# Kernel tuning notes

Hardware: AMD Instinct MI355X
Metric: run time of the kernel (lower is better)

## Reference

```python
import jax, jax.numpy as jnp
import numpy as np

B, N, D, H, DK, MS, FF = 8, 256, 256, 16, 16, 16, 512
EPS = 1e-5


def _inorm(x, scale, bias):
    # InstanceNorm1d over the node dim (axis=1) per channel, affine
    m = jnp.mean(x, axis=1, keepdims=True)
    v = jnp.var(x, axis=1, keepdims=True)
    return (x - m) * jax.lax.rsqrt(v + EPS) * scale + bias


def _heads(x):
    b, n, _ = x.shape
    return x.reshape(b, n, H, DK).transpose(0, 2, 1, 3)  # (b,H,n,DK)


def _block(emb_r, emb_c, cost, Wq, Wk, Wv, m1w, m1b, m2w, m2b, cw, cb,
           n1s, n1b, w1, b1, w2, b2, n2s, n2b):
    b, n, _ = emb_r.shape
    q = _heads(emb_r @ Wq)
    k = _heads(emb_c @ Wk)
    v = _heads(emb_c @ Wv)
    dot = jnp.einsum('bhid,bhjd->bhij', q, k) / jnp.sqrt(jnp.float32(DK))
    # stack dot-product score with cost-matrix score: (b,H,r,c,2)
    two = jnp.stack([dot, jnp.broadcast_to(cost[:, None], dot.shape)], axis=-1)
    # per-head 2 -> MS -> 1 MLP on each (row,col) score pair
    ms1 = jax.nn.relu(jnp.einsum('bhrcs,hsm->bhrcm', two, m1w)
                      + m1b[None, :, None, None, :])
    mixed = jnp.einsum('bhrcm,hm->bhrc', ms1, m2w[:, :, 0]) \
            + m2b[:, 0][None, :, None, None]
    w = jax.nn.softmax(mixed, axis=-1)
    out = jnp.einsum('bhrc,bhcd->bhrd', w, v)
    out_concat = out.transpose(0, 2, 1, 3).reshape(b, n, H * DK)
    mh = out_concat @ cw + cb
    out1 = _inorm(emb_r + mh, n1s, n1b)
    ff = jax.nn.relu(out1 @ w1 + b1) @ w2 + b2
    return _inorm(out1 + ff, n2s, n2b)


def setup_inputs() -> dict:
    key = jax.random.key(0)
    keys = iter(jax.random.split(key, 64))
    def nrm(shape, s=0.05):
        return jax.random.normal(next(keys), shape, dtype=jnp.float32) * s
    inp = {
        'row_emb': nrm((B, N, D), 1.0),
        'col_emb': nrm((B, N, D), 1.0),
        'cost_mat': jax.random.uniform(next(keys), (B, N, N), dtype=jnp.float32),
    }
    for p in ('r', 'c'):
        inp[p + 'Wq'] = nrm((D, H * DK)); inp[p + 'Wk'] = nrm((D, H * DK)); inp[p + 'Wv'] = nrm((D, H * DK))
        inp[p + 'm1w'] = nrm((H, 2, MS), 0.5); inp[p + 'm1b'] = nrm((H, MS), 0.5)
        inp[p + 'm2w'] = nrm((H, MS, 1), 0.25); inp[p + 'm2b'] = nrm((H, 1), 0.25)
        inp[p + 'cw'] = nrm((H * DK, D)); inp[p + 'cb'] = jnp.zeros((D,), jnp.float32)
        inp[p + 'n1s'] = jnp.ones((D,), jnp.float32); inp[p + 'n1b'] = jnp.zeros((D,), jnp.float32)
        inp[p + 'w1'] = nrm((D, FF)); inp[p + 'b1'] = jnp.zeros((FF,), jnp.float32)
        inp[p + 'w2'] = nrm((FF, D)); inp[p + 'b2'] = jnp.zeros((D,), jnp.float32)
        inp[p + 'n2s'] = jnp.ones((D,), jnp.float32); inp[p + 'n2b'] = jnp.zeros((D,), jnp.float32)
    return inp


def reference(row_emb, col_emb, cost_mat,
              rWq, rWk, rWv, rm1w, rm1b, rm2w, rm2b, rcw, rcb,
              rn1s, rn1b, rw1, rb1, rw2, rb2, rn2s, rn2b,
              cWq, cWk, cWv, cm1w, cm1b, cm2w, cm2b, ccw, ccb,
              cn1s, cn1b, cw1, cb1, cw2, cb2, cn2s, cn2b):
    row_out = _block(row_emb, col_emb, cost_mat,
                     rWq, rWk, rWv, rm1w, rm1b, rm2w, rm2b, rcw, rcb,
                     rn1s, rn1b, rw1, rb1, rw2, rb2, rn2s, rn2b)
    col_out = _block(col_emb, row_emb, cost_mat.transpose(0, 2, 1),
                     cWq, cWk, cWv, cm1w, cm1b, cm2w, cm2b, ccw, ccb,
                     cn1s, cn1b, cw1, cb1, cw2, cb2, cn2s, cn2b)
    return row_out, col_out
```

## Files before the change

kernel.cpp:

```cpp
#include <hip/hip_runtime.h>
#include <hip/hip_bf16.h>
#include <hip/hip_fp16.h>

#define Bc 8
#define Nc 256
#define Dc 256
#define Hc 16
#define DKc 16
#define MSc 16
#define FFc 512
#define SZc 524288
#define WHALF 524288
#define FFH 1048576

typedef __hip_bfloat16 bf16;
typedef __attribute__((ext_vector_type(8))) short bfrag8;
typedef __attribute__((ext_vector_type(4))) float f32x4;

__device__ __forceinline__ short f2bs(float x) {
    bf16 t = __float2bfloat16(x);
    return *reinterpret_cast<short*>(&t);
}

__device__ __forceinline__ short f2hs(float x) {
    __half t = __float2half(x);
    return *reinterpret_cast<short*>(&t);
}

__device__ __forceinline__ __half2 pk_relu(__half2 x) {
    __half2 r;
    asm("v_pk_max_f16 %0, %1, 0" : "=v"(r) : "v"(x));
    return r;
}

__global__ void setup_kernel(const float* __restrict__ e0, const float* __restrict__ e1,
                             bf16* __restrict__ o0, bf16* __restrict__ o1,
                             float* __restrict__ statsB,
                             const float* __restrict__ cost,
                             short* __restrict__ costH, short* __restrict__ costHT,
                             const float* rWq, const float* rWk, const float* rWv,
                             const float* rcw, const float* rw1, const float* rw2,
                             const float* cWq, const float* cWk, const float* cWv,
                             const float* ccw, const float* cw1, const float* cw2,
                             const float* rm1w, const float* rm1b, const float* rm2w,
                             const float* cm1w, const float* cm1b, const float* cm2w,
                             __half2* __restrict__ Wpk,
                             bf16* __restrict__ WT) {
    int y = blockIdx.y;
    if (y < 2) {
        const float* src = y ? e1 : e0;
        bf16* dst = y ? o1 : o0;
        size_t base = (size_t)blockIdx.x * 2048 + threadIdx.x;
#pragma unroll
        for (int i = 0; i < 8; ++i)
            dst[base + i * 256] = __float2bfloat16(src[base + i * 256]);
        return;
    }
    if (y == 2) {
        if (blockIdx.x < 64) {
            statsB[blockIdx.x * 256 + threadIdx.x] = 0.f;
        } else if (blockIdx.x < 66) {
            int p = blockIdx.x - 64;
            const float* m1w = p ? cm1w : rm1w;
            const float* m1b = p ? cm1b : rm1b;
            const float* m2w = p ? cm2w : rm2w;
            int h = threadIdx.x >> 4, m = threadIdx.x & 15;
            __half2* wp = Wpk + (size_t)(p * 16 + h) * 64;
            wp[m]      = __float2half2_rn(m1w[h * 32 + m] * 0.25f);
            wp[16 + m] = __float2half2_rn(m1w[h * 32 + 16 + m]);
            wp[32 + m] = __float2half2_rn(m1b[h * 16 + m]);
            wp[48 + m] = __float2half2_rn(m2w[h * 16 + m]);
        }
        return;
    }
    if (y == 15) {
        size_t base = (size_t)blockIdx.x * 2048 + threadIdx.x;
#pragma unroll
        for (int i = 0; i < 8; ++i)
            costH[base + i * 256] = f2hs(cost[base + i * 256]);
        return;
    }
    __shared__ float t[32][33];
    int tx = threadIdx.x & 31, ty = threadIdx.x >> 5;
    if (y >= 16) {
        int tl = blockIdx.x + (y - 16) * 256;
        int bb = tl >> 6, t2 = tl & 63;
        int r0 = (t2 >> 3) * 32, c0 = (t2 & 7) * 32;
        const float* src = cost + (size_t)bb * 65536;
        short* dst = costHT + (size_t)bb * 65536;
#pragma unroll
        for (int i = 0; i < 4; ++i)
            t[ty + i * 8][tx] = src[(size_t)(r0 + ty + i * 8) * 256 + c0 + tx];
        __syncthreads();
#pragma unroll
        for (int i = 0; i < 4; ++i)
            dst[(size_t)(c0 + ty + i * 8) * 256 + r0 + tx] = f2hs(t[tx][ty + i * 8]);
        return;
    }
    int z = y - 3;
    int p = z / 6, widx = z % 6;
    const float* src; int K, N; size_t off;
    switch (widx) {
        case 0: src = p ? cWq : rWq; K = 256; N = 256; off = 0; break;
        case 1: src = p ? cWk : rWk; K = 256; N = 256; off = 65536; break;
        case 2: src = p ? cWv : rWv; K = 256; N = 256; off = 131072; break;
        case 3: src = p ? ccw : rcw; K = 256; N = 256; off = 196608; break;
        case 4: src = p ? cw1 : rw1; K = 256; N = 512; off = 262144; break;
        default: src = p ? cw2 : rw2; K = 512; N = 256; off = 393216; break;
    }
    int Ntiles = N >> 5, Ktiles = K >> 5;
    if ((int)blockIdx.x >= Ktiles * Ntiles) return;
    int kt = blockIdx.x / Ntiles, nt = blockIdx.x - kt * Ntiles;
    int k0 = kt * 32, n0 = nt * 32;
    bf16* dst = WT + (size_t)p * WHALF + off;
#pragma unroll
    for (int i = 0; i < 4; ++i)
        t[ty + i * 8][tx] = src[(size_t)(k0 + ty + i * 8) * N + n0 + tx];
    __syncthreads();
#pragma unroll
    for (int i = 0; i < 4; ++i)
        dst[(size_t)(n0 + ty + i * 8) * K + k0 + tx] = __float2bfloat16(t[tx][ty + i * 8]);
}

__global__ void gemm_qkv_kernel(const short* __restrict__ embRb, const short* __restrict__ embCb,
                                const short* __restrict__ WT, bf16* __restrict__ qkv) {
    int z = blockIdx.z;
    int p = z / 3, j = z % 3;
    const short* A  = (j == 0) ? (p ? embCb : embRb) : (p ? embRb : embCb);
    const short* BT = WT + (size_t)p * WHALF + j * 65536;
    bf16* out = qkv + (size_t)z * SZc;

    int lane = threadIdx.x & 63, w = threadIdx.x >> 6;
    int m_base = blockIdx.x * 64 + (w & 1) * 32;
    int n_base = blockIdx.y * 64 + (w >> 1) * 32;
    int mr = lane & 15, quad = lane >> 4;

    const short* pa0 = A + (size_t)(m_base + mr) * 256 + quad * 8;
    const short* pa1 = pa0 + 16 * 256;
    const short* pb0 = BT + (size_t)(n_base + mr) * 256 + quad * 8;
    const short* pb1 = pb0 + 16 * 256;

    f32x4 acc00 = {0.f, 0.f, 0.f, 0.f}, acc01 = {0.f, 0.f, 0.f, 0.f};
    f32x4 acc10 = {0.f, 0.f, 0.f, 0.f}, acc11 = {0.f, 0.f, 0.f, 0.f};
#pragma unroll
    for (int kt = 0; kt < 256; kt += 32) {
        bfrag8 A0 = *(const bfrag8*)(pa0 + kt);
        bfrag8 A1 = *(const bfrag8*)(pa1 + kt);
        bfrag8 B0 = *(const bfrag8*)(pb0 + kt);
        bfrag8 B1 = *(const bfrag8*)(pb1 + kt);
        acc00 = __builtin_amdgcn_mfma_f32_16x16x32_bf16(A0, B0, acc00, 0, 0, 0);
        acc01 = __builtin_amdgcn_mfma_f32_16x16x32_bf16(A0, B1, acc01, 0, 0, 0);
        acc10 = __builtin_amdgcn_mfma_f32_16x16x32_bf16(A1, B0, acc10, 0, 0, 0);
        acc11 = __builtin_amdgcn_mfma_f32_16x16x32_bf16(A1, B1, acc11, 0, 0, 0);
    }

#pragma unroll
    for (int jt = 0; jt < 2; ++jt) {
        int col = n_base + jt * 16 + mr;
        int h = col >> 4, dk = col & 15;
        f32x4 a0 = jt ? acc01 : acc00;
        f32x4 a1 = jt ? acc11 : acc10;
#pragma unroll
        for (int r = 0; r < 4; ++r) {
            int row0 = m_base + quad * 4 + r;
            int row1 = row0 + 16;
            int b0 = row0 >> 8, n0 = row0 & 255;
            int b1 = row1 >> 8, n1 = row1 & 255;
            out[((size_t)(b0 * Hc + h) * Nc + n0) * DKc + dk] = __float2bfloat16(a0[r]);
            out[((size_t)(b1 * Hc + h) * Nc + n1) * DKc + dk] = __float2bfloat16(a1[r]);
        }
    }
}

__global__ void attn_kernel(const short* __restrict__ qkv,
                            const short* __restrict__ costH,
                            const short* __restrict__ costHT,
                            const __half2* __restrict__ Wpk,
                            const float* rm2b, const float* cm2b,
                            bf16* __restrict__ attnb) {
    int b = blockIdx.x, h = blockIdx.y;
    int p = blockIdx.z >> 4, rc = blockIdx.z & 15;
    const short* Q = qkv + (size_t)(p * 3 + 0) * SZc;
    const short* K = qkv + (size_t)(p * 3 + 1) * SZc;
    const short* V = qkv + (size_t)(p * 3 + 2) * SZc;
    const __half2* wp = Wpk + (size_t)(p * 16 + h) * 64;
    float b2v = (p ? cm2b : rm2b)[h];
    bf16* out_concat = attnb + (size_t)p * SZc;

    int bh = b * Hc + h;
    int r0 = rc * 16;
    int c = threadIdx.x;
    int lane = c & 63, wid = c >> 6;
    int mr = lane & 15, quad = lane >> 4;

    __shared__ __align__(16) short sVT[16 * 264];
    __shared__ __align__(16) short sEb[16 * 264];
    __shared__ float sPart[4 * 256];
    __shared__ float sSum[16 * 4];

    {
        const short* vp = V + ((size_t)bh * Nc + c) * DKc;
        bfrag8 v0 = *(const bfrag8*)vp;
        bfrag8 v1 = *(const bfrag8*)(vp + 8);
#pragma unroll
        for (int i = 0; i < 8; ++i) {
            sVT[i * 264 + c]       = v0[i];
            sVT[(8 + i) * 264 + c] = v1[i];
        }
    }

    bfrag8 qf = {0, 0, 0, 0, 0, 0, 0, 0};
    if (quad < 2)
        qf = *(const bfrag8*)(Q + ((size_t)bh * Nc + r0 + mr) * DKc + quad * 8);

    __half2 sv2[8];
#pragma unroll
    for (int t = 0; t < 4; ++t) {
        bfrag8 kf = {0, 0, 0, 0, 0, 0, 0, 0};
        if (quad < 2)
            kf = *(const bfrag8*)(K + ((size_t)bh * Nc + wid * 64 + t * 16 + mr) * DKc + quad * 8);
        f32x4 acc = {0.f, 0.f, 0.f, 0.f};
        acc = __builtin_amdgcn_mfma_f32_16x16x32_bf16(qf, kf, acc, 0, 0, 0);
        sv2[t * 2]     = __floats2half2_rn(acc[0], acc[1]);
        sv2[t * 2 + 1] = __floats2half2_rn(acc[2], acc[3]);
    }

    const __half2* cp = (const __half2*)((p ? costH : costHT) + (size_t)b * 65536);
    __half2 cv2[8];
#pragma unroll
    for (int t = 0; t < 4; ++t) {
        int col = wid * 64 + t * 16 + mr;
        int h2i = (col << 7) + (r0 >> 1) + (quad << 1);
        uint2 u = *(const uint2*)(cp + h2i);
        cv2[t * 2]     = *reinterpret_cast<__half2*>(&u.x);
        cv2[t * 2 + 1] = *reinterpret_cast<__half2*>(&u.y);
    }

    __syncthreads();

    const __half2 z2 = __half2half2(__float2half(0.f));
    __half2 mix2[8] = {z2, z2, z2, z2, z2, z2, z2, z2};
#pragma unroll
    for (int m = 0; m < MSc; ++m) {
        __half2 w1d = wp[m];
        __half2 w1c = wp[16 + m];
        __half2 b1v = wp[32 + m];
        __half2 w2v = wp[48 + m];
#pragma unroll
        for (int s = 0; s < 8; ++s) {
            __half2 tt = __hfma2(sv2[s], w1d, __hfma2(cv2[s], w1c, b1v));
            mix2[s] = __hfma2(pk_relu(tt), w2v, mix2[s]);
        }
    }
    float ex[16];
#pragma unroll
    for (int s = 0; s < 8; ++s) {
        float2 mf = __half22float2(mix2[s]);
        ex[s * 2]     = __expf(mf.x + b2v);
        ex[s * 2 + 1] = __expf(mf.y + b2v);
    }

#pragma unroll
    for (int t = 0; t < 4; ++t)
#pragma unroll
        for (int r = 0; r < 4; ++r)
            sEb[(quad * 4 + r) * 264 + wid * 64 + t * 16 + mr] = f2bs(ex[t * 4 + r]);

#pragma unroll
    for (int r = 0; r < 4; ++r) {
        float rp = ex[r] + ex[4 + r] + ex[8 + r] + ex[12 + r];
        rp += __shfl_xor(rp, 1);
        rp += __shfl_xor(rp, 2);
        rp += __shfl_xor(rp, 4);
        rp += __shfl_xor(rp, 8);
        if (mr == 0) sSum[(quad * 4 + r) * 4 + wid] = rp;
    }
    __syncthreads();

    {
        const short* pa = &sEb[mr * 264 + wid * 64 + quad * 8];
        const short* pb = &sVT[mr * 264 + wid * 64 + quad * 8];
        f32x4 acc = {0.f, 0.f, 0.f, 0.f};
        bfrag8 a0 = *(const bfrag8*)pa;
        bfrag8 b0 = *(const bfrag8*)pb;
        acc = __builtin_amdgcn_mfma_f32_16x16x32_bf16(a0, b0, acc, 0, 0, 0);
        bfrag8 a1 = *(const bfrag8*)(pa + 32);
        bfrag8 b1 = *(const bfrag8*)(pb + 32);
        acc = __builtin_amdgcn_mfma_f32_16x16x32_bf16(a1, b1, acc, 0, 0, 0);
#pragma unroll
        for (int r = 0; r < 4; ++r)
            sPart[wid * 256 + (quad * 4 + r) * 16 + mr] = acc[r];
    }
    __syncthreads();

    {
        int r = c >> 4, dk = c & 15;
        float o = sPart[c] + sPart[256 + c] + sPart[512 + c] + sPart[768 + c];
        float sum = sSum[r * 4] + sSum[r * 4 + 1] + sSum[r * 4 + 2] + sSum[r * 4 + 3];
        out_concat[((size_t)(b * Nc + r0 + r)) * Dc + h * DKc + dk] =
            __float2bfloat16(o / sum);
    }
}

__global__ void gemm_cat_kernel(const short* __restrict__ attnb, const short* __restrict__ WT,
                                const float* rcb, const float* ccb,
                                const float* __restrict__ resR, const float* __restrict__ resC,
                                float* __restrict__ x1, float* __restrict__ stats1) {
    int p = blockIdx.z;
    const short* A  = attnb + (size_t)p * SZc;
    const short* BT = WT + (size_t)p * WHALF + 196608;
    const float* bias = p ? ccb : rcb;
    const float* res  = p ? resC : resR;
    float* outF = x1 + (size_t)p * SZc;
    float* st   = stats1 + p * 4096;

    int lane = threadIdx.x & 63, w = threadIdx.x >> 6;
    int m_base = blockIdx.x * 64 + (w & 1) * 32;
    int n_base = blockIdx.y * 64 + (w >> 1) * 32;
    int mr = lane & 15, quad = lane >> 4;

    const short* pa0 = A + (size_t)(m_base + mr) * 256 + quad * 8;
    const short* pa1 = pa0 + (size_t)16 * 256;
    const short* pb0 = BT + (size_t)(n_base + mr) * 256 + quad * 8;
    const short* pb1 = pb0 + (size_t)16 * 256;

    f32x4 acc00 = {0.f, 0.f, 0.f, 0.f}, acc01 = {0.f, 0.f, 0.f, 0.f};
    f32x4 acc10 = {0.f, 0.f, 0.f, 0.f}, acc11 = {0.f, 0.f, 0.f, 0.f};
#pragma unroll
    for (int kt = 0; kt < 256; kt += 32) {
        bfrag8 A0 = *(const bfrag8*)(pa0 + kt);
        bfrag8 A1 = *(const bfrag8*)(pa1 + kt);
        bfrag8 B0 = *(const bfrag8*)(pb0 + kt);
        bfrag8 B1 = *(const bfrag8*)(pb1 + kt);
        acc00 = __builtin_amdgcn_mfma_f32_16x16x32_bf16(A0, B0, acc00, 0, 0, 0);
        acc01 = __builtin_amdgcn_mfma_f32_16x16x32_bf16(A0, B1, acc01, 0, 0, 0);
        acc10 = __builtin_amdgcn_mfma_f32_16x16x32_bf16(A1, B0, acc10, 0, 0, 0);
        acc11 = __builtin_amdgcn_mfma_f32_16x16x32_bf16(A1, B1, acc11, 0, 0, 0);
    }

    int bb = m_base >> 8;
#pragma unroll
    for (int jt = 0; jt < 2; ++jt) {
        int col = n_base + jt * 16 + mr;
        float bv = bias[col];
        f32x4 a0 = jt ? acc01 : acc00;
        f32x4 a1 = jt ? acc11 : acc10;
        float ssum = 0.f, ssq = 0.f;
#pragma unroll
        for (int r = 0; r < 4; ++r) {
            int row0 = m_base + quad * 4 + r;
            int row1 = row0 + 16;
            float v0 = a0[r] + bv + res[(size_t)row0 * 256 + col];
            float v1 = a1[r] + bv + res[(size_t)row1 * 256 + col];
            outF[(size_t)row0 * 256 + col] = v0;
            outF[(size_t)row1 * 256 + col] = v1;
            ssum += v0 + v1;
            ssq  += v0 * v0 + v1 * v1;
        }
        atomicAdd(&st[(bb * 256 + col) * 2],     ssum);
        atomicAdd(&st[(bb * 256 + col) * 2 + 1], ssq);
    }
}

__global__ __launch_bounds__(256) void gemm_ff1n_kernel(
        const float* __restrict__ x1, const float* __restrict__ stats1,
        const float* rn1s, const float* rn1b, const float* cn1s, const float* cn1b,
        const short* __restrict__ WT, const float* rb1, const float* cb1,
        bf16* __restrict__ ffh) {
    int p = blockIdx.z;
    const float* X   = x1 + (size_t)p * SZc;
    const float* st  = stats1 + p * 4096;
    const float* n1s = p ? cn1s : rn1s;
    const float* n1b = p ? cn1b : rn1b;
    const short* BT  = WT + (size_t)p * WHALF + 262144;
    const float* bias = p ? cb1 : rb1;
    bf16* outB = ffh + (size_t)p * FFH;

    __shared__ __align__(16) short sA[64 * 264];
    int c = threadIdx.x;
    int m_base = blockIdx.x * 64;
    int b = m_base >> 8;

    float s = st[(b * 256 + c) * 2];
    float q = st[(b * 256 + c) * 2 + 1];
    float mean = s * (1.f / Nc);
    float var = q * (1.f / Nc) - mean * mean;
    float inv = rsqrtf(var + 1e-5f) * n1s[c];
    float nb = n1b[c];
#pragma unroll 8
    for (int i = 0; i < 64; ++i) {
        float v = X[(size_t)(m_base + i) * 256 + c];
        sA[i * 264 + c] = f2bs((v - mean) * inv + nb);
    }
    __syncthreads();

    int lane = c & 63, w = c >> 6;
    int mloc = (w & 1) * 32;
    int n_base = blockIdx.y * 64 + (w >> 1) * 32;
    int mr = lane & 15, quad = lane >> 4;

    const short* pa0 = &sA[(mloc + mr) * 264 + quad * 8];
    const short* pa1 = pa0 + 16 * 264;
    const short* pb0 = BT + (size_t)(n_base + mr) * 256 + quad * 8;
    const short* pb1 = pb0 + 16 * 256;

    f32x4 acc00 = {0.f, 0.f, 0.f, 0.f}, acc01 = {0.f, 0.f, 0.f, 0.f};
    f32x4 acc10 = {0.f, 0.f, 0.f, 0.f}, acc11 = {0.f, 0.f, 0.f, 0.f};
#pragma unroll
    for (int kt = 0; kt < 256; kt += 32) {
        bfrag8 A0 = *(const bfrag8*)(pa0 + kt);
        bfrag8 A1 = *(const bfrag8*)(pa1 + kt);
        bfrag8 B0 = *(const bfrag8*)(pb0 + kt);
        bfrag8 B1 = *(const bfrag8*)(pb1 + kt);
        acc00 = __builtin_amdgcn_mfma_f32_16x16x32_bf16(A0, B0, acc00, 0, 0, 0);
        acc01 = __builtin_amdgcn_mfma_f32_16x16x32_bf16(A0, B1, acc01, 0, 0, 0);
        acc10 = __builtin_amdgcn_mfma_f32_16x16x32_bf16(A1, B0, acc10, 0, 0, 0);
        acc11 = __builtin_amdgcn_mfma_f32_16x16x32_bf16(A1, B1, acc11, 0, 0, 0);
    }

#pragma unroll
    for (int jt = 0; jt < 2; ++jt) {
        int col = n_base + jt * 16 + mr;
        float bv = bias[col];
        f32x4 a0 = jt ? acc01 : acc00;
        f32x4 a1 = jt ? acc11 : acc10;
#pragma unroll
        for (int r = 0; r < 4; ++r) {
            int row0 = m_base + mloc + quad * 4 + r;
            int row1 = row0 + 16;
            outB[(size_t)row0 * 512 + col] = __float2bfloat16(fmaxf(a0[r] + bv, 0.f));
            outB[(size_t)row1 * 512 + col] = __float2bfloat16(fmaxf(a1[r] + bv, 0.f));
        }
    }
}

__global__ void gemm_ff2n_kernel(const short* __restrict__ ffh, const short* __restrict__ WT,
                                 const float* rb2, const float* cb2,
                                 const float* __restrict__ x1, const float* __restrict__ stats1,
                                 const float* rn1s, const float* rn1b,
                                 const float* cn1s, const float* cn1b,
                                 float* __restrict__ ff2, float* __restrict__ stats2) {
    int p = blockIdx.z;
    const short* A  = ffh + (size_t)p * FFH;
    const short* BT = WT + (size_t)p * WHALF + 393216;
    const float* bias = p ? cb2 : rb2;
    const float* X   = x1 + (size_t)p * SZc;
    const float* st1 = stats1 + p * 4096;
    const float* n1s = p ? cn1s : rn1s;
    const float* n1b = p ? cn1b : rn1b;
    float* outF = ff2 + (size_t)p * SZc;
    float* st2  = stats2 + p * 4096;

    int lane = threadIdx.x & 63, w = threadIdx.x >> 6;
    int m_base = blockIdx.x * 64 + (w & 1) * 32;
    int n_base = blockIdx.y * 64 + (w >> 1) * 32;
    int mr = lane & 15, quad = lane >> 4;

    const short* pa0 = A + (size_t)(m_base + mr) * 512 + quad * 8;
    const short* pa1 = pa0 + (size_t)16 * 512;
    const short* pb0 = BT + (size_t)(n_base + mr) * 512 + quad * 8;
    const short* pb1 = pb0 + (size_t)16 * 512;

    f32x4 acc00 = {0.f, 0.f, 0.f, 0.f}, acc01 = {0.f, 0.f, 0.f, 0.f};
    f32x4 acc10 = {0.f, 0.f, 0.f, 0.f}, acc11 = {0.f, 0.f, 0.f, 0.f};
#pragma unroll
    for (int kt = 0; kt < 512; kt += 32) {
        bfrag8 A0 = *(const bfrag8*)(pa0 + kt);
        bfrag8 A1 = *(const bfrag8*)(pa1 + kt);
        bfrag8 B0 = *(const bfrag8*)(pb0 + kt);
        bfrag8 B1 = *(const bfrag8*)(pb1 + kt);
        acc00 = __builtin_amdgcn_mfma_f32_16x16x32_bf16(A0, B0, acc00, 0, 0, 0);
        acc01 = __builtin_amdgcn_mfma_f32_16x16x32_bf16(A0, B1, acc01, 0, 0, 0);
        acc10 = __builtin_amdgcn_mfma_f32_16x16x32_bf16(A1, B0, acc10, 0, 0, 0);
        acc11 = __builtin_amdgcn_mfma_f32_16x16x32_bf16(A1, B1, acc11, 0, 0, 0);
    }

    int bb = m_base >> 8;
#pragma unroll
    for (int jt = 0; jt < 2; ++jt) {
        int col = n_base + jt * 16 + mr;
        float s1 = st1[(bb * 256 + col) * 2];
        float q1 = st1[(bb * 256 + col) * 2 + 1];
        float mean1 = s1 * (1.f / Nc);
        float var1 = q1 * (1.f / Nc) - mean1 * mean1;
        float inv1 = rsqrtf(var1 + 1e-5f) * n1s[col];
        float nb1 = n1b[col];
        float bv = bias[col];
        f32x4 a0 = jt ? acc01 : acc00;
        f32x4 a1 = jt ? acc11 : acc10;
        float ssum = 0.f, ssq = 0.f;
#pragma unroll
        for (int r = 0; r < 4; ++r) {
            int row0 = m_base + quad * 4 + r;
            int row1 = row0 + 16;
            float res0 = (X[(size_t)row0 * 256 + col] - mean1) * inv1 + nb1;
            float res1 = (X[(size_t)row1 * 256 + col] - mean1) * inv1 + nb1;
            float v0 = a0[r] + bv + res0;
            float v1 = a1[r] + bv + res1;
            outF[(size_t)row0 * 256 + col] = v0;
            outF[(size_t)row1 * 256 + col] = v1;
            ssum += v0 + v1;
            ssq  += v0 * v0 + v1 * v1;
        }
        atomicAdd(&st2[(bb * 256 + col) * 2],     ssum);
        atomicAdd(&st2[(bb * 256 + col) * 2 + 1], ssq);
    }
}

__global__ void apply_kernel(const float* __restrict__ x, const float* __restrict__ stats,
                             const float* sR, const float* bR,
                             const float* sC, const float* bC,
                             float* __restrict__ outF) {
    int p = blockIdx.y;
    int t = threadIdx.x;
    int row = blockIdx.x * 4 + (t >> 6);
    int d0 = (t & 63) * 4;
    int b = row >> 8;
    const float* st = stats + p * 4096 + (size_t)(b * 256 + d0) * 2;
    float4 s01 = *(const float4*)st;
    float4 s23 = *(const float4*)(st + 4);
    const float* sp = p ? sC : sR;
    const float* bp = p ? bC : bR;
    float4 sc = *(const float4*)(sp + d0);
    float4 bi = *(const float4*)(bp + d0);
    float4 v = *(const float4*)(x + (size_t)p * SZc + (size_t)row * Dc + d0);
    float sums[4] = {s01.x, s01.z, s23.x, s23.z};
    float sqs[4]  = {s01.y, s01.w, s23.y, s23.w};
    float vv[4]   = {v.x, v.y, v.z, v.w};
    float scs[4]  = {sc.x, sc.y, sc.z, sc.w};
    float bis[4]  = {bi.x, bi.y, bi.z, bi.w};
    float4 o;
#pragma unroll
    for (int j = 0; j < 4; ++j) {
        float mean = sums[j] * (1.f / Nc);
        float var = sqs[j] * (1.f / Nc) - mean * mean;
        float inv = rsqrtf(var + 1e-5f);
        ((float*)&o)[j] = (vv[j] - mean) * inv * scs[j] + bis[j];
    }
    *(float4*)(outF + (size_t)p * SZc + (size_t)row * Dc + d0) = o;
}

extern "C" void kernel_launch(void* const* d_in, const int* in_sizes, int n_in,
                              void* d_out, int out_size, void* d_ws, size_t ws_size,
                              hipStream_t stream) {
    const float* row_emb = (const float*)d_in[0];
    const float* col_emb = (const float*)d_in[1];
    const float* cost    = (const float*)d_in[2];
    float* out = (float*)d_out;
    float* ws = (float*)d_ws;
#define RP(i) ((const float*)d_in[3 + (i)])
#define CP(i) ((const float*)d_in[20 + (i)])

    float* x1     = ws;
    float* ff2    = ws + 2 * (size_t)SZc;
    float* statsB = ws + 4 * (size_t)SZc;
    __half2* Wpk  = (__half2*)(statsB + 16384);
    bf16* bfbase  = (bf16*)(Wpk + 4096);
    bf16* qkvb  = bfbase;
    bf16* embRb = qkvb + 6 * (size_t)SZc;
    bf16* embCb = embRb + SZc;
    bf16* attnb = embCb + SZc;
    bf16* ffh   = attnb + 2 * (size_t)SZc;
    bf16* WT    = ffh + 4 * (size_t)SZc;
    short* costH  = (short*)(WT + 2 * (size_t)WHALF);
    short* costHT = costH + SZc;
    float* stats1 = statsB;
    float* stats2 = statsB + 8192;

    setup_kernel<<<dim3(256, 18), 256, 0, stream>>>(
        row_emb, col_emb, embRb, embCb, statsB,
        cost, costH, costHT,
        RP(0), RP(1), RP(2), RP(7), RP(11), RP(13),
        CP(0), CP(1), CP(2), CP(7), CP(11), CP(13),
        RP(3), RP(4), RP(5), CP(3), CP(4), CP(5), Wpk, WT);
    gemm_qkv_kernel<<<dim3(32, 4, 6), 256, 0, stream>>>(
        (const short*)embRb, (const short*)embCb, (const short*)WT, qkvb);
    attn_kernel<<<dim3(Bc, Hc, 32), 256, 0, stream>>>(
        (const short*)qkvb, costH, costHT, Wpk, RP(6), CP(6), attnb);
    gemm_cat_kernel<<<dim3(32, 4, 2), 256, 0, stream>>>(
        (const short*)attnb, (const short*)WT, RP(8), CP(8), row_emb, col_emb, x1, stats1);
    gemm_ff1n_kernel<<<dim3(32, 8, 2), 256, 0, stream>>>(
        x1, stats1, RP(9), RP(10), CP(9), CP(10),
        (const short*)WT, RP(12), CP(12), ffh);
    gemm_ff2n_kernel<<<dim3(32, 4, 2), 256, 0, stream>>>(
        (const short*)ffh, (const short*)WT, RP(14), CP(14),
        x1, stats1, RP(9), RP(10), CP(9), CP(10), ff2, stats2);
    apply_kernel<<<dim3(512, 2), 256, 0, stream>>>(
        ff2, stats2, RP(15), RP(16), CP(15), CP(16), out);
#undef RP
#undef CP
}
```

Before: 205.9 us.

## Skew row/col block pipelines and co-launch independent stages in merged kernels

Splits each stage into its row (p=0) and column (p=1) halves and staggers them, so every launch runs one pipeline's stage N alongside the other pipeline's stage N-1. Blocks pick a stage body from a virtual block index, letting small GEMM grids share a launch with heavier attention or FF work. The goal is to fill idle compute units and cut the tail of under-occupied launches. The cost is one extra launch, a larger shared-memory allocation for the merged kernels, and heterogeneous blocks within a grid.

```diff
diff --git a/kernel.cpp b/kernel.cpp
--- a/kernel.cpp
+++ b/kernel.cpp
@@ -122,17 +122,16 @@
         dst[(size_t)(n0 + ty + i * 8) * K + k0 + tx] = __float2bfloat16(t[tx][ty + i * 8]);
 }
 
-__global__ void gemm_qkv_kernel(const short* __restrict__ embRb, const short* __restrict__ embCb,
-                                const short* __restrict__ WT, bf16* __restrict__ qkv) {
-    int z = blockIdx.z;
-    int p = z / 3, j = z % 3;
+__device__ __forceinline__ void qkv_body(int p, int j, int vbx, int vby,
+        const short* __restrict__ embRb, const short* __restrict__ embCb,
+        const short* __restrict__ WT, bf16* __restrict__ qkv) {
     const short* A  = (j == 0) ? (p ? embCb : embRb) : (p ? embRb : embCb);
     const short* BT = WT + (size_t)p * WHALF + j * 65536;
-    bf16* out = qkv + (size_t)z * SZc;
+    bf16* out = qkv + (size_t)(p * 3 + j) * SZc;
 
     int lane = threadIdx.x & 63, w = threadIdx.x >> 6;
-    int m_base = blockIdx.x * 64 + (w & 1) * 32;
-    int n_base = blockIdx.y * 64 + (w >> 1) * 32;
+    int m_base = vbx * 64 + (w & 1) * 32;
+    int n_base = vby * 64 + (w >> 1) * 32;
     int mr = lane & 15, quad = lane >> 4;
 
     const short* pa0 = A + (size_t)(m_base + mr) * 256 + quad * 8;
@@ -172,14 +171,17 @@
     }
 }
 
-__global__ void attn_kernel(const short* __restrict__ qkv,
-                            const short* __restrict__ costH,
-                            const short* __restrict__ costHT,
-                            const __half2* __restrict__ Wpk,
-                            const float* rm2b, const float* cm2b,
-                            bf16* __restrict__ attnb) {
-    int b = blockIdx.x, h = blockIdx.y;
-    int p = blockIdx.z >> 4, rc = blockIdx.z & 15;
+#define ATTN_SMEM 21504
+__device__ __forceinline__ void attn_body(int p, int b, int h, int rc, char* smem,
+        const short* __restrict__ qkv,
+        const short* __restrict__ costH, const short* __restrict__ costHT,
+        const __half2* __restrict__ Wpk,
+        const float* rm2b, const float* cm2b, bf16* __restrict__ attnb) {
+    short* sVT  = (short*)smem;
+    short* sEb  = (short*)(smem + 8448);
+    float* sPart = (float*)(smem + 16896);
+    float* sSum  = (float*)(smem + 20992);
+
     const short* Q = qkv + (size_t)(p * 3 + 0) * SZc;
     const short* K = qkv + (size_t)(p * 3 + 1) * SZc;
     const short* V = qkv + (size_t)(p * 3 + 2) * SZc;
@@ -192,11 +194,6 @@
     int c = threadIdx.x;
     int lane = c & 63, wid = c >> 6;
     int mr = lane & 15, quad = lane >> 4;
-
-    __shared__ __align__(16) short sVT[16 * 264];
-    __shared__ __align__(16) short sEb[16 * 264];
-    __shared__ float sPart[4 * 256];
-    __shared__ float sSum[16 * 4];
 
     {
         const short* vp = V + ((size_t)bh * Nc + c) * DKc;
@@ -302,11 +299,11 @@
     }
 }
 
-__global__ void gemm_cat_kernel(const short* __restrict__ attnb, const short* __restrict__ WT,
-                                const float* rcb, const float* ccb,
-                                const float* __restrict__ resR, const float* __restrict__ resC,
-                                float* __restrict__ x1, float* __restrict__ stats1) {
-    int p = blockIdx.z;
+__device__ __forceinline__ void cat_body(int p, int vbx, int vby,
+        const short* __restrict__ attnb, const short* __restrict__ WT,
+        const float* rcb, const float* ccb,
+        const float* __restrict__ resR, const float* __restrict__ resC,
+        float* __restrict__ x1, float* __restrict__ stats1) {
     const short* A  = attnb + (size_t)p * SZc;
     const short* BT = WT + (size_t)p * WHALF + 196608;
     const float* bias = p ? ccb : rcb;
@@ -315,8 +312,8 @@
     float* st   = stats1 + p * 4096;
 
     int lane = threadIdx.x & 63, w = threadIdx.x >> 6;
-    int m_base = blockIdx.x * 64 + (w & 1) * 32;
-    int n_base = blockIdx.y * 64 + (w >> 1) * 32;
+    int m_base = vbx * 64 + (w & 1) * 32;
+    int n_base = vby * 64 + (w >> 1) * 32;
     int mr = lane & 15, quad = lane >> 4;
 
     const short* pa0 = A + (size_t)(m_base + mr) * 256 + quad * 8;
@@ -362,12 +359,13 @@
     }
 }
 
-__global__ __launch_bounds__(256) void gemm_ff1n_kernel(
+#define FF1N_SMEM 33792
+__device__ __forceinline__ void ff1n_body(int p, int vbx, int vby, char* smem,
         const float* __restrict__ x1, const float* __restrict__ stats1,
         const float* rn1s, const float* rn1b, const float* cn1s, const float* cn1b,
         const short* __restrict__ WT, const float* rb1, const float* cb1,
         bf16* __restrict__ ffh) {
-    int p = blockIdx.z;
+    short* sA = (short*)smem;
     const float* X   = x1 + (size_t)p * SZc;
     const float* st  = stats1 + p * 4096;
     const float* n1s = p ? cn1s : rn1s;
@@ -376,9 +374,8 @@
     const float* bias = p ? cb1 : rb1;
     bf16* outB = ffh + (size_t)p * FFH;
 
-    __shared__ __align__(16) short sA[64 * 264];
     int c = threadIdx.x;
-    int m_base = blockIdx.x * 64;
+    int m_base = vbx * 64;
     int b = m_base >> 8;
 
     float s = st[(b * 256 + c) * 2];
@@ -396,7 +393,7 @@
 
     int lane = c & 63, w = c >> 6;
     int mloc = (w & 1) * 32;
-    int n_base = blockIdx.y * 64 + (w >> 1) * 32;
+    int n_base = vby * 64 + (w >> 1) * 32;
     int mr = lane & 15, quad = lane >> 4;
 
     const short* pa0 = &sA[(mloc + mr) * 264 + quad * 8];
@@ -434,13 +431,13 @@
     }
 }
 
-__global__ void gemm_ff2n_kernel(const short* __restrict__ ffh, const short* __restrict__ WT,
-                                 const float* rb2, const float* cb2,
-                                 const float* __restrict__ x1, const float* __restrict__ stats1,
-                                 const float* rn1s, const float* rn1b,
-                                 const float* cn1s, const float* cn1b,
-                                 float* __restrict__ ff2, float* __restrict__ stats2) {
-    int p = blockIdx.z;
+__device__ __forceinline__ void ff2n_body(int p, int vbx, int vby,
+        const short* __restrict__ ffh, const short* __restrict__ WT,
+        const float* rb2, const float* cb2,
+        const float* __restrict__ x1, const float* __restrict__ stats1,
+        const float* rn1s, const float* rn1b,
+        const float* cn1s, const float* cn1b,
+        float* __restrict__ ff2, float* __restrict__ stats2) {
     const short* A  = ffh + (size_t)p * FFH;
     const short* BT = WT + (size_t)p * WHALF + 393216;
     const float* bias = p ? cb2 : rb2;
@@ -452,8 +449,8 @@
     float* st2  = stats2 + p * 4096;
 
     int lane = threadIdx.x & 63, w = threadIdx.x >> 6;
-    int m_base = blockIdx.x * 64 + (w & 1) * 32;
-    int n_base = blockIdx.y * 64 + (w >> 1) * 32;
+    int m_base = vbx * 64 + (w & 1) * 32;
+    int n_base = vby * 64 + (w >> 1) * 32;
     int mr = lane & 15, quad = lane >> 4;
 
     const short* pa0 = A + (size_t)(m_base + mr) * 512 + quad * 8;
@@ -507,13 +504,13 @@
     }
 }
 
-__global__ void apply_kernel(const float* __restrict__ x, const float* __restrict__ stats,
-                             const float* sR, const float* bR,
-                             const float* sC, const float* bC,
-                             float* __restrict__ outF) {
-    int p = blockIdx.y;
+__device__ __forceinline__ void apply_body(int p, int vb,
+        const float* __restrict__ x, const float* __restrict__ stats,
+        const float* sR, const float* bR,
+        const float* sC, const float* bC,
+        float* __restrict__ outF) {
     int t = threadIdx.x;
-    int row = blockIdx.x * 4 + (t >> 6);
+    int row = vb * 4 + (t >> 6);
     int d0 = (t & 63) * 4;
     int b = row >> 8;
     const float* st = stats + p * 4096 + (size_t)(b * 256 + d0) * 2;
@@ -540,6 +537,102 @@
     *(float4*)(outF + (size_t)p * SZc + (size_t)row * Dc + d0) = o;
 }
 
+__global__ __launch_bounds__(256) void k_qkv0(
+        const short* embRb, const short* embCb, const short* WT, bf16* qkv) {
+    int vb = blockIdx.x;
+    qkv_body(0, vb >> 7, vb & 31, (vb >> 5) & 3, embRb, embCb, WT, qkv);
+}
+
+__global__ __launch_bounds__(256) void k_attn0_qkv1(
+        const short* qkv, const short* costH, const short* costHT,
+        const __half2* Wpk, const float* rm2b, const float* cm2b, bf16* attnb,
+        const short* embRb, const short* embCb, const short* WT, bf16* qkvout) {
+    __shared__ __align__(16) char smem[ATTN_SMEM];
+    int vb = blockIdx.x;
+    if (vb < 2048)
+        attn_body(0, vb & 7, (vb >> 3) & 15, vb >> 7, smem,
+                  qkv, costH, costHT, Wpk, rm2b, cm2b, attnb);
+    else {
+        int u = vb - 2048;
+        qkv_body(1, u >> 7, u & 31, (u >> 5) & 3, embRb, embCb, WT, qkvout);
+    }
+}
+
+__global__ __launch_bounds__(256) void k_attn1_cat0(
+        const short* qkv, const short* costH, const short* costHT,
+        const __half2* Wpk, const float* rm2b, const float* cm2b, bf16* attnb,
+        const short* WT, const float* rcb, const float* ccb,
+        const float* resR, const float* resC, float* x1, float* stats1) {
+    __shared__ __align__(16) char smem[ATTN_SMEM];
+    int vb = blockIdx.x;
+    if (vb < 2048)
+        attn_body(1, vb & 7, (vb >> 3) & 15, vb >> 7, smem,
+                  qkv, costH, costHT, Wpk, rm2b, cm2b, attnb);
+    else {
+        int u = vb - 2048;
+        cat_body(0, u & 31, u >> 5, (const short*)attnb, WT, rcb, ccb,
+                 resR, resC, x1, stats1);
+    }
+}
+
+__global__ __launch_bounds__(256) void k_ff1n0_cat1(
+        const float* x1, const float* stats1,
+        const float* rn1s, const float* rn1b, const float* cn1s, const float* cn1b,
+        const short* WT, const float* rb1, const float* cb1, bf16* ffh,
+        const short* attnb, const float* rcb, const float* ccb,
+        const float* resR, const float* resC, float* x1out, float* stats1out) {
+    __shared__ __align__(16) char smem[FF1N_SMEM];
+    int vb = blockIdx.x;
+    if (vb < 256)
+        ff1n_body(0, vb & 31, vb >> 5, smem, x1, stats1,
+                  rn1s, rn1b, cn1s, cn1b, WT, rb1, cb1, ffh);
+    else {
+        int u = vb - 256;
+        cat_body(1, u & 31, u >> 5, attnb, WT, rcb, ccb, resR, resC,
+                 x1out, stats1out);
+    }
+}
+
+__global__ __launch_bounds__(256) void k_ff2n0_ff1n1(
+        const short* ffh, const short* WT, const float* rb2, const float* cb2,
+        const float* x1, const float* stats1,
+        const float* rn1s, const float* rn1b, const float* cn1s, const float* cn1b,
+        float* ff2, float* stats2,
+        const float* rb1, const float* cb1, bf16* ffhout) {
+    __shared__ __align__(16) char smem[FF1N_SMEM];
+    int vb = blockIdx.x;
+    if (vb < 128)
+        ff2n_body(0, vb & 31, vb >> 5, ffh, WT, rb2, cb2, x1, stats1,
+                  rn1s, rn1b, cn1s, cn1b, ff2, stats2);
+    else {
+        int u = vb - 128;
+        ff1n_body(1, u & 31, u >> 5, smem, x1, stats1,
+                  rn1s, rn1b, cn1s, cn1b, WT, rb1, cb1, ffhout);
+    }
+}
+
+__global__ __launch_bounds__(256) void k_ff2n1_apply0(
+        const short* ffh, const short* WT, const float* rb2, const float* cb2,
+        const float* x1, const float* stats1,
+        const float* rn1s, const float* rn1b, const float* cn1s, const float* cn1b,
+        float* ff2, float* stats2,
+        const float* n2sR, const float* n2bR, const float* n2sC, const float* n2bC,
+        float* outF) {
+    int vb = blockIdx.x;
+    if (vb < 128)
+        ff2n_body(1, vb & 31, vb >> 5, ffh, WT, rb2, cb2, x1, stats1,
+                  rn1s, rn1b, cn1s, cn1b, ff2, stats2);
+    else
+        apply_body(0, vb - 128, ff2, stats2, n2sR, n2bR, n2sC, n2bC, outF);
+}
+
+__global__ __launch_bounds__(256) void k_apply1(
+        const float* ff2, const float* stats2,
+        const float* n2sR, const float* n2bR, const float* n2sC, const float* n2bC,
+        float* outF) {
+    apply_body(1, blockIdx.x, ff2, stats2, n2sR, n2bR, n2sC, n2bC, outF);
+}
+
 extern "C" void kernel_launch(void* const* d_in, const int* in_sizes, int n_in,
                               void* d_out, int out_size, void* d_ws, size_t ws_size,
                               hipStream_t stream) {
@@ -573,19 +666,27 @@
         RP(0), RP(1), RP(2), RP(7), RP(11), RP(13),
         CP(0), CP(1), CP(2), CP(7), CP(11), CP(13),
         RP(3), RP(4), RP(5), CP(3), CP(4), CP(5), Wpk, WT);
-    gemm_qkv_kernel<<<dim3(32, 4, 6), 256, 0, stream>>>(
+    k_qkv0<<<384, 256, 0, stream>>>(
         (const short*)embRb, (const short*)embCb, (const short*)WT, qkvb);
-    attn_kernel<<<dim3(Bc, Hc, 32), 256, 0, stream>>>(
-        (const short*)qkvb, costH, costHT, Wpk, RP(6), CP(6), attnb);
-    gemm_cat_kernel<<<dim3(32, 4, 2), 256, 0, stream>>>(
-        (const short*)attnb, (const short*)WT, RP(8), CP(8), row_emb, col_emb, x1, stats1);
-    gemm_ff1n_kernel<<<dim3(32, 8, 2), 256, 0, stream>>>(
+    k_attn0_qkv1<<<2432, 256, 0, stream>>>(
+        (const short*)qkvb, costH, costHT, Wpk, RP(6), CP(6), attnb,
+        (const short*)embRb, (const short*)embCb, (const short*)WT, qkvb);
+    k_attn1_cat0<<<2176, 256, 0, stream>>>(
+        (const short*)qkvb, costH, costHT, Wpk, RP(6), CP(6), attnb,
+        (const short*)WT, RP(8), CP(8), row_emb, col_emb, x1, stats1);
+    k_ff1n0_cat1<<<384, 256, 0, stream>>>(
         x1, stats1, RP(9), RP(10), CP(9), CP(10),
-        (const short*)WT, RP(12), CP(12), ffh);
-    gemm_ff2n_kernel<<<dim3(32, 4, 2), 256, 0, stream>>>(
+        (const short*)WT, RP(12), CP(12), ffh,
+        (const short*)attnb, RP(8), CP(8), row_emb, col_emb, x1, stats1);
+    k_ff2n0_ff1n1<<<384, 256, 0, stream>>>(
         (const short*)ffh, (const short*)WT, RP(14), CP(14),
-        x1, stats1, RP(9), RP(10), CP(9), CP(10), ff2, stats2);
-    apply_kernel<<<dim3(512, 2), 256, 0, stream>>>(
+        x1, stats1, RP(9), RP(10), CP(9), CP(10), ff2, stats2,
+        RP(12), CP(12), ffh);
+    k_ff2n1_apply0<<<640, 256, 0, stream>>>(
+        (const short*)ffh, (const short*)WT, RP(14), CP(14),
+        x1, stats1, RP(9), RP(10), CP(9), CP(10), ff2, stats2,
+        RP(15), RP(16), CP(15), CP(16), out);
+    k_apply1<<<512, 256, 0, stream>>>(
         ff2, stats2, RP(15), RP(16), CP(15), CP(16), out);
 #undef RP
 #undef CP
```

After: 227.4 us. 1.1x slower.
